# Kernel tuning notes

Hardware: AMD Instinct MI355X
Metric: run time of the kernel (lower is better)

Reference implementation:

```python
import jax, jax.numpy as jnp
import numpy as np

N = 100000
E = 1600000
D_IN, D_HID, D_OUT = 64, 64, 64
NEG_SLOPE = 0.2
EPS = 1e-16


def _gat_layer(x, W, att_src, att_dst, bias, src, dst, n_nodes):
    """Single-head PyG GATConv, add_self_loops=False."""
    h = x @ W                                  # [N, out]
    a_s = h @ att_src                          # [N] per-node source score
    a_d = h @ att_dst                          # [N] per-node dest score
    e = jax.nn.leaky_relu(a_s[src] + a_d[dst], NEG_SLOPE)   # [E]
    # softmax over incoming edges of each dst node
    m = jax.ops.segment_max(e, dst, num_segments=n_nodes)    # [N]
    ex = jnp.exp(e - m[dst])                                  # [E]
    denom = jax.ops.segment_sum(ex, dst, num_segments=n_nodes)  # [N]
    alpha = ex / (denom[dst] + EPS)                            # [E]
    # weighted scatter-aggregate of source features to dst
    out = jax.ops.segment_sum(h[src] * alpha[:, None], dst, num_segments=n_nodes)
    return out + bias


def setup_inputs() -> dict:
    key = jax.random.key(0)
    ks = jax.random.split(key, 10)
    x = jax.random.normal(ks[0], (N, D_IN), dtype=jnp.float32)
    edge_index = jax.random.randint(ks[1], (2, E), 0, N, dtype=jnp.int32)
    s1 = 1.0 / np.sqrt(D_IN)
    s2 = 1.0 / np.sqrt(D_HID)
    return {
        "x": x,
        "edge_index": edge_index,
        "W1": jax.random.normal(ks[2], (D_IN, D_HID), dtype=jnp.float32) * s1,
        "att_src1": jax.random.normal(ks[3], (D_HID,), dtype=jnp.float32) * s2,
        "att_dst1": jax.random.normal(ks[4], (D_HID,), dtype=jnp.float32) * s2,
        "b1": jnp.zeros((D_HID,), dtype=jnp.float32),
        "W2": jax.random.normal(ks[5], (D_HID, D_OUT), dtype=jnp.float32) * s2,
        "att_src2": jax.random.normal(ks[6], (D_OUT,), dtype=jnp.float32) * (1.0 / np.sqrt(D_OUT)),
        "att_dst2": jax.random.normal(ks[7], (D_OUT,), dtype=jnp.float32) * (1.0 / np.sqrt(D_OUT)),
        "b2": jnp.zeros((D_OUT,), dtype=jnp.float32),
    }


def reference(x, edge_index, W1, att_src1, att_dst1, b1, W2, att_src2, att_dst2, b2):
    src, dst = edge_index[0], edge_index[1]
    h = _gat_layer(x, W1, att_src1, att_dst1, b1, src, dst, N)
    h = jax.nn.relu(h)
    # dropout(p=0.2) is identity in eval mode
    out = _gat_layer(h, W2, att_src2, att_dst2, b2, src, dst, N)
    return out
```

## Files before the change

### kernel.cpp

```cpp
#include <hip/hip_runtime.h>

#define N_NODES 100000
#define N_EDGES 1600000
#define D 64
#define NEG_SLOPE 0.2f
#define SM_EPS 1e-16f

#define BSHIFT 9
#define BSIZE (1 << BSHIFT)
#define NB ((N_NODES + BSIZE - 1) >> BSHIFT)
#define PAD 16
#define TPB 256
#define EPT 16
#define TILE (TPB * EPT)
#define NWG_E ((N_EDGES + TILE - 1) / TILE)
#define CSR_CAP 10240

#define GEMM_RR 8
#define GEMM_ROWS 128
#define NWG_GEMM ((N_NODES + GEMM_ROWS - 1) / GEMM_ROWS)

#define COMP(v, kk) ((kk) == 0 ? (v).x : (kk) == 1 ? (v).y : (kk) == 2 ? (v).z : (v).w)

typedef _Float16 half4_t __attribute__((ext_vector_type(4)));


__global__ __launch_bounds__(TPB) void k_bhist(const int* __restrict__ dst,
                                               int* __restrict__ gbh) {
    __shared__ int hist[NB];
    int t = threadIdx.x;
    for (int i = t; i < NB; i += TPB) hist[i] = 0;
    __syncthreads();
    int base = blockIdx.x * TILE;
#pragma unroll
    for (int j = 0; j < EPT; j++) {
        int i = base + j * TPB + t;
        if (i < N_EDGES) atomicAdd(&hist[dst[i] >> BSHIFT], 1);
    }
    __syncthreads();
    for (int i = t; i < NB; i += TPB)
        if (hist[i]) atomicAdd(&gbh[i * PAD], hist[i]);
}

__global__ __launch_bounds__(256) void k_scan_nb(const int* __restrict__ gbh,
                                                 int* __restrict__ bbase,
                                                 int* __restrict__ bcur) {
    __shared__ int lds[256];
    int t = threadIdx.x;
    int v = (t < NB) ? gbh[t * PAD] : 0;
    lds[t] = v;
    __syncthreads();
    for (int s = 1; s < 256; s <<= 1) {
        int a = (t >= s) ? lds[t - s] : 0;
        __syncthreads();
        lds[t] += a;
        __syncthreads();
    }
    int excl = lds[t] - v;
    if (t < NB) { bbase[t] = excl; bcur[t * PAD] = excl; }
    if (t == 0) bbase[NB] = N_EDGES;
}

__global__ __launch_bounds__(TPB) void k_bscatter(const int* __restrict__ src,
                                                  const int* __restrict__ dst,
                                                  int* __restrict__ bcur,
                                                  unsigned* __restrict__ ebuf) {
    __shared__ int hist[NB];
    __shared__ int cursor[NB];
    __shared__ int lbase[NB];
    __shared__ int tsum[TPB];
    __shared__ unsigned stage[TILE];
    __shared__ int stageaddr[TILE];
    int t = threadIdx.x;
    for (int i = t; i < NB; i += TPB) hist[i] = 0;
    __syncthreads();
    int base = blockIdx.x * TILE;
#pragma unroll
    for (int j = 0; j < EPT; j++) {
        int i = base + j * TPB + t;
        if (i < N_EDGES) atomicAdd(&hist[dst[i] >> BSHIFT], 1);
    }
    __syncthreads();
    int v = (t < NB) ? hist[t] : 0;
    tsum[t] = v;
    __syncthreads();
    for (int s = 1; s < 256; s <<= 1) {
        int a = (t >= s) ? tsum[t - s] : 0;
        __syncthreads();
        tsum[t] += a;
        __syncthreads();
    }
    int excl = tsum[t] - v;
    if (t < NB) {
        int gb = v ? atomicAdd(&bcur[t * PAD], v) : 0;
        lbase[t] = gb - excl;
        cursor[t] = excl;
    }
    __syncthreads();
#pragma unroll
    for (int j = 0; j < EPT; j++) {
        int i = base + j * TPB + t;
        if (i < N_EDGES) {
            int d = dst[i];
            int b = d >> BSHIFT;
            int r = atomicAdd(&cursor[b], 1);
            stage[r] = (unsigned)src[i] | ((unsigned)(d & (BSIZE - 1)) << 17);
            stageaddr[r] = lbase[b] + r;
        }
    }
    __syncthreads();
    int total = min(TILE, N_EDGES - base);
    for (int s = t; s < total; s += TPB) ebuf[stageaddr[s]] = stage[s];
}

__global__ __launch_bounds__(TPB) void k_bcsr(const int* __restrict__ bbase,
                                              const unsigned* __restrict__ ebuf,
                                              int* __restrict__ off,
                                              int* __restrict__ csr) {
    __shared__ int dh[BSIZE];
    __shared__ int dl[BSIZE];
    __shared__ int tsum[TPB];
    __shared__ int stage[CSR_CAP];
    int b = blockIdx.x;
    int t = threadIdx.x;
    int beg = bbase[b], end = bbase[b + 1];
    int cnt = end - beg;
    dh[t] = 0; dh[t + TPB] = 0;
    __syncthreads();
    for (int i = beg + t; i < end; i += TPB)
        atomicAdd(&dh[(ebuf[i] >> 17) & (BSIZE - 1)], 1);
    __syncthreads();
    int v0 = dh[2 * t], v1 = dh[2 * t + 1];
    tsum[t] = v0 + v1;
    __syncthreads();
    for (int s = 1; s < 256; s <<= 1) {
        int a = (t >= s) ? tsum[t - s] : 0;
        __syncthreads();
        tsum[t] += a;
        __syncthreads();
    }
    int excl = tsum[t] - (v0 + v1);
    dl[2 * t] = excl;
    dl[2 * t + 1] = excl + v0;
    int gd = (b << BSHIFT) + 2 * t;
    if (gd < N_NODES) off[gd] = beg + excl;
    if (gd + 1 < N_NODES) off[gd + 1] = beg + excl + v0;
    if (b == 0 && t == 0) off[N_NODES] = N_EDGES;
    dh[2 * t] = 0; dh[2 * t + 1] = 0;
    __syncthreads();
    if (cnt <= CSR_CAP) {
        for (int i = beg + t; i < end; i += TPB) {
            unsigned pk = ebuf[i];
            int ld = (pk >> 17) & (BSIZE - 1);
            int r = atomicAdd(&dh[ld], 1);
            stage[dl[ld] + r] = (int)(pk & 0x1FFFFu);
        }
        __syncthreads();
        for (int s = t; s < cnt; s += TPB) csr[beg + s] = stage[s];
    } else {
        for (int i = beg + t; i < end; i += TPB) {
            unsigned pk = ebuf[i];
            int ld = (pk >> 17) & (BSIZE - 1);
            int r = atomicAdd(&dh[ld], 1);
            csr[beg + dl[ld] + r] = (int)(pk & 0x1FFFFu);
        }
    }
}


__global__ __launch_bounds__(256) void k_wvec(
    const float* __restrict__ W1, const float* __restrict__ as1,
    const float* __restrict__ ad1, const float* __restrict__ W2,
    const float* __restrict__ as2, const float* __restrict__ ad2,
    float* __restrict__ wv) {
    int w = threadIdx.x >> 6, lane = threadIdx.x & 63;
    const float* W  = (w < 2) ? W1 : W2;
    const float* av = (w == 0) ? as1 : (w == 1) ? ad1 : (w == 2) ? as2 : ad2;
    const float4* Wr = (const float4*)(W + lane * D);
    const float4* a4 = (const float4*)av;
    float acc0 = 0.f, acc1 = 0.f;
#pragma unroll
    for (int c = 0; c < D / 8; c++) {
        float4 w0 = Wr[2 * c], w1 = Wr[2 * c + 1];
        float4 v0 = a4[2 * c], v1 = a4[2 * c + 1];
        acc0 += w0.x * v0.x + w0.y * v0.y + w0.z * v0.z + w0.w * v0.w;
        acc1 += w1.x * v1.x + w1.y * v1.y + w1.z * v1.z + w1.w * v1.w;
    }
    wv[w * D + lane] = acc0 + acc1;
}

__global__ __launch_bounds__(256) void k_gemm(
    const float* __restrict__ x, const float* __restrict__ W,
    const float* __restrict__ wv,
    _Float16* __restrict__ h16, float* __restrict__ a_s,
    float* __restrict__ a_d) {
    __shared__ float4 Wl4[D * D / 4];
    __shared__ float4 wvs[D / 4], wvd[D / 4];
    int t = threadIdx.x;
    const float4* W4 = (const float4*)W;
#pragma unroll
    for (int i = 0; i < 4; i++) Wl4[i * 256 + t] = W4[i * 256 + t];
    if (t < D / 4) wvs[t] = ((const float4*)wv)[t];
    else if (t < D / 2) wvd[t - D / 4] = ((const float4*)(wv + D))[t - D / 4];
    __syncthreads();
    int q = t & 15;
    int r0 = blockIdx.x * GEMM_ROWS + (t >> 4) * GEMM_RR;
    const float4* x4 = (const float4*)x;
    float4 acc[GEMM_RR];
    float sa[GEMM_RR], ea[GEMM_RR];
#pragma unroll
    for (int j = 0; j < GEMM_RR; j++) {
        acc[j] = {0.f, 0.f, 0.f, 0.f};
        sa[j] = 0.f; ea[j] = 0.f;
    }
    for (int k4 = 0; k4 < D / 4; k4++) {
        float4 ws4 = wvs[k4], wd4 = wvd[k4];
        float4 xv[GEMM_RR];
#pragma unroll
        for (int j = 0; j < GEMM_RR; j++) {
            int r = r0 + j;
            r = (r < N_NODES) ? r : N_NODES - 1;
            xv[j] = x4[(size_t)r * (D / 4) + k4];
        }
#pragma unroll
        for (int j = 0; j < GEMM_RR; j++) {
            sa[j] += xv[j].x * ws4.x + xv[j].y * ws4.y +
                     xv[j].z * ws4.z + xv[j].w * ws4.w;
            ea[j] += xv[j].x * wd4.x + xv[j].y * wd4.y +
                     xv[j].z * wd4.z + xv[j].w * wd4.w;
        }
#pragma unroll
        for (int kk = 0; kk < 4; kk++) {
            float4 w4 = Wl4[(k4 * 4 + kk) * 16 + q];
#pragma unroll
            for (int j = 0; j < GEMM_RR; j++) {
                float xs = COMP(xv[j], kk);
                acc[j].x = fmaf(xs, w4.x, acc[j].x);
                acc[j].y = fmaf(xs, w4.y, acc[j].y);
                acc[j].z = fmaf(xs, w4.z, acc[j].z);
                acc[j].w = fmaf(xs, w4.w, acc[j].w);
            }
        }
    }
#pragma unroll
    for (int j = 0; j < GEMM_RR; j++) {
        int r = r0 + j;
        if (r < N_NODES) {
            half4_t hh = {(_Float16)acc[j].x, (_Float16)acc[j].y,
                          (_Float16)acc[j].z, (_Float16)acc[j].w};
            *(half4_t*)(h16 + (size_t)r * D + q * 4) = hh;
            if (q == 0) { a_s[r] = sa[j]; a_d[r] = ea[j]; }
        }
    }
}

__global__ __launch_bounds__(256) void k_aggr(
    const int* __restrict__ off, const int* __restrict__ csr,
    const _Float16* __restrict__ h16, const float* __restrict__ a_s,
    const float* __restrict__ a_d, const float* __restrict__ bias,
    float* __restrict__ out, int do_relu) {
    int node = (blockIdx.x * blockDim.x + threadIdx.x) >> 4;
    int q = threadIdx.x & 15;
    if (node >= N_NODES) return;
    int beg = off[node], end = off[node + 1];
    float ad = a_d[node];
    float s = 0.f;
    float4 acc = {0.f, 0.f, 0.f, 0.f};
    for (int c = beg; c < end; c += 8) {
        int v[8];
        float w[8];
        half4_t hv[8];
#pragma unroll
        for (int i = 0; i < 8; i++) {
            int idx = c + i;
            v[i] = (idx < end) ? csr[idx] : csr[beg];
        }
#pragma unroll
        for (int i = 0; i < 8; i++)
            hv[i] = *(const half4_t*)(h16 + (size_t)v[i] * D + q * 4);
#pragma unroll
        for (int i = 0; i < 8; i++) {
            float tv = a_s[v[i]] + ad;
            tv = fmaxf(tv, NEG_SLOPE * tv);
            w[i] = (c + i < end) ? __expf(tv) : 0.f;
        }
#pragma unroll
        for (int i = 0; i < 8; i++) {
            s += w[i];
            acc.x = fmaf(w[i], (float)hv[i].x, acc.x);
            acc.y = fmaf(w[i], (float)hv[i].y, acc.y);
            acc.z = fmaf(w[i], (float)hv[i].z, acc.z);
            acc.w = fmaf(w[i], (float)hv[i].w, acc.w);
        }
    }
    float inv = 1.f / (s + SM_EPS);
    float4 b4 = ((const float4*)bias)[q];
    float4 o;
    o.x = fmaf(acc.x, inv, b4.x);
    o.y = fmaf(acc.y, inv, b4.y);
    o.z = fmaf(acc.z, inv, b4.z);
    o.w = fmaf(acc.w, inv, b4.w);
    if (do_relu) {
        o.x = fmaxf(o.x, 0.f); o.y = fmaxf(o.y, 0.f);
        o.z = fmaxf(o.z, 0.f); o.w = fmaxf(o.w, 0.f);
    }
    ((float4*)(out + (size_t)node * D))[q] = o;
}


extern "C" void kernel_launch(void* const* d_in, const int* in_sizes, int n_in,
                              void* d_out, int out_size, void* d_ws, size_t ws_size,
                              hipStream_t stream) {
    const float* x   = (const float*)d_in[0];
    const int*   ei  = (const int*)d_in[1];
    const float* W1  = (const float*)d_in[2];
    const float* as1 = (const float*)d_in[3];
    const float* ad1 = (const float*)d_in[4];
    const float* b1  = (const float*)d_in[5];
    const float* W2  = (const float*)d_in[6];
    const float* as2 = (const float*)d_in[7];
    const float* ad2 = (const float*)d_in[8];
    const float* b2  = (const float*)d_in[9];
    float* out = (float*)d_out;

    const int* src = ei;
    const int* dst = ei + N_EDGES;

    char* ws = (char*)d_ws;
    size_t o = 0;
    auto alloc = [&](size_t bytes) { void* p = ws + o; o += (bytes + 255) & ~255ull; return p; };
    _Float16* h16 = (_Float16*)alloc((size_t)N_NODES * D * sizeof(_Float16));
    float* a_s   = (float*)alloc(N_NODES * sizeof(float));
    float* a_d   = (float*)alloc(N_NODES * sizeof(float));
    int*   off   = (int*)alloc((N_NODES + 1) * sizeof(int));
    int*   csr   = (int*)alloc(N_EDGES * sizeof(int));
    int*   gbh   = (int*)alloc(NB * PAD * sizeof(int));
    int*   bbase = (int*)alloc((NB + 1) * sizeof(int));
    int*   bcur  = (int*)alloc(NB * PAD * sizeof(int));
    float* wv    = (float*)alloc(4 * D * sizeof(float));
    unsigned* ebuf = (unsigned*)h16;

    k_wvec<<<1, 256, 0, stream>>>(W1, as1, ad1, W2, as2, ad2, wv);

    hipMemsetAsync(gbh, 0, NB * PAD * sizeof(int), stream);
    k_bhist   <<<NWG_E, TPB, 0, stream>>>(dst, gbh);
    k_scan_nb <<<1, 256, 0, stream>>>(gbh, bbase, bcur);
    k_bscatter<<<NWG_E, TPB, 0, stream>>>(src, dst, bcur, ebuf);
    k_bcsr    <<<NB, TPB, 0, stream>>>(bbase, ebuf, off, csr);

    k_gemm<<<NWG_GEMM, 256, 0, stream>>>(x, W1, wv, h16, a_s, a_d);
    k_aggr<<<(N_NODES * 16 + 255) / 256, 256, 0, stream>>>(off, csr, h16, a_s, a_d, b1, out, 1);

    k_gemm<<<NWG_GEMM, 256, 0, stream>>>(out, W2, wv + 2 * D, h16, a_s, a_d);
    k_aggr<<<(N_NODES * 16 + 255) / 256, 256, 0, stream>>>(off, csr, h16, a_s, a_d, b2, out, 0);
}
```

Before: 278.4 us.

## Fuse layer-1 GEMM with edge histogram and widen CSR build blocks

The layer-1 GEMM and the destination-bucket histogram now run in one launch, with block ranges split between the two tasks. The separate attention-vector kernel goes away: each GEMM block computes W·att itself from the W tile already in shared memory. ebuf gets its own workspace buffer instead of aliasing h16, and the scatter and CSR kernels move from 256 to 512 threads per block. The aim is fewer launches and overlap of independent front-end work, at the cost of extra workspace memory and some redundant per-block dot products.

```diff
diff --git a/kernel.cpp b/kernel.cpp
--- a/kernel.cpp
+++ b/kernel.cpp
@@ -11,6 +11,7 @@
 #define NB ((N_NODES + BSIZE - 1) >> BSHIFT)
 #define PAD 16
 #define TPB 256
+#define TPB2 512
 #define EPT 16
 #define TILE (TPB * EPT)
 #define NWG_E ((N_EDGES + TILE - 1) / TILE)
@@ -24,188 +25,38 @@
 
 typedef _Float16 half4_t __attribute__((ext_vector_type(4)));
 
-
-__global__ __launch_bounds__(TPB) void k_bhist(const int* __restrict__ dst,
-                                               int* __restrict__ gbh) {
-    __shared__ int hist[NB];
-    int t = threadIdx.x;
-    for (int i = t; i < NB; i += TPB) hist[i] = 0;
-    __syncthreads();
-    int base = blockIdx.x * TILE;
-#pragma unroll
-    for (int j = 0; j < EPT; j++) {
-        int i = base + j * TPB + t;
-        if (i < N_EDGES) atomicAdd(&hist[dst[i] >> BSHIFT], 1);
-    }
-    __syncthreads();
-    for (int i = t; i < NB; i += TPB)
-        if (hist[i]) atomicAdd(&gbh[i * PAD], hist[i]);
-}
-
-__global__ __launch_bounds__(256) void k_scan_nb(const int* __restrict__ gbh,
-                                                 int* __restrict__ bbase,
-                                                 int* __restrict__ bcur) {
-    __shared__ int lds[256];
-    int t = threadIdx.x;
-    int v = (t < NB) ? gbh[t * PAD] : 0;
-    lds[t] = v;
-    __syncthreads();
-    for (int s = 1; s < 256; s <<= 1) {
-        int a = (t >= s) ? lds[t - s] : 0;
-        __syncthreads();
-        lds[t] += a;
-        __syncthreads();
-    }
-    int excl = lds[t] - v;
-    if (t < NB) { bbase[t] = excl; bcur[t * PAD] = excl; }
-    if (t == 0) bbase[NB] = N_EDGES;
-}
-
-__global__ __launch_bounds__(TPB) void k_bscatter(const int* __restrict__ src,
-                                                  const int* __restrict__ dst,
-                                                  int* __restrict__ bcur,
-                                                  unsigned* __restrict__ ebuf) {
-    __shared__ int hist[NB];
-    __shared__ int cursor[NB];
-    __shared__ int lbase[NB];
-    __shared__ int tsum[TPB];
-    __shared__ unsigned stage[TILE];
-    __shared__ int stageaddr[TILE];
-    int t = threadIdx.x;
-    for (int i = t; i < NB; i += TPB) hist[i] = 0;
-    __syncthreads();
-    int base = blockIdx.x * TILE;
-#pragma unroll
-    for (int j = 0; j < EPT; j++) {
-        int i = base + j * TPB + t;
-        if (i < N_EDGES) atomicAdd(&hist[dst[i] >> BSHIFT], 1);
-    }
-    __syncthreads();
-    int v = (t < NB) ? hist[t] : 0;
-    tsum[t] = v;
-    __syncthreads();
-    for (int s = 1; s < 256; s <<= 1) {
-        int a = (t >= s) ? tsum[t - s] : 0;
-        __syncthreads();
-        tsum[t] += a;
-        __syncthreads();
-    }
-    int excl = tsum[t] - v;
-    if (t < NB) {
-        int gb = v ? atomicAdd(&bcur[t * PAD], v) : 0;
-        lbase[t] = gb - excl;
-        cursor[t] = excl;
-    }
-    __syncthreads();
-#pragma unroll
-    for (int j = 0; j < EPT; j++) {
-        int i = base + j * TPB + t;
-        if (i < N_EDGES) {
-            int d = dst[i];
-            int b = d >> BSHIFT;
-            int r = atomicAdd(&cursor[b], 1);
-            stage[r] = (unsigned)src[i] | ((unsigned)(d & (BSIZE - 1)) << 17);
-            stageaddr[r] = lbase[b] + r;
-        }
-    }
-    __syncthreads();
-    int total = min(TILE, N_EDGES - base);
-    for (int s = t; s < total; s += TPB) ebuf[stageaddr[s]] = stage[s];
-}
-
-__global__ __launch_bounds__(TPB) void k_bcsr(const int* __restrict__ bbase,
-                                              const unsigned* __restrict__ ebuf,
-                                              int* __restrict__ off,
-                                              int* __restrict__ csr) {
-    __shared__ int dh[BSIZE];
-    __shared__ int dl[BSIZE];
-    __shared__ int tsum[TPB];
-    __shared__ int stage[CSR_CAP];
-    int b = blockIdx.x;
-    int t = threadIdx.x;
-    int beg = bbase[b], end = bbase[b + 1];
-    int cnt = end - beg;
-    dh[t] = 0; dh[t + TPB] = 0;
-    __syncthreads();
-    for (int i = beg + t; i < end; i += TPB)
-        atomicAdd(&dh[(ebuf[i] >> 17) & (BSIZE - 1)], 1);
-    __syncthreads();
-    int v0 = dh[2 * t], v1 = dh[2 * t + 1];
-    tsum[t] = v0 + v1;
-    __syncthreads();
-    for (int s = 1; s < 256; s <<= 1) {
-        int a = (t >= s) ? tsum[t - s] : 0;
-        __syncthreads();
-        tsum[t] += a;
-        __syncthreads();
-    }
-    int excl = tsum[t] - (v0 + v1);
-    dl[2 * t] = excl;
-    dl[2 * t + 1] = excl + v0;
-    int gd = (b << BSHIFT) + 2 * t;
-    if (gd < N_NODES) off[gd] = beg + excl;
-    if (gd + 1 < N_NODES) off[gd + 1] = beg + excl + v0;
-    if (b == 0 && t == 0) off[N_NODES] = N_EDGES;
-    dh[2 * t] = 0; dh[2 * t + 1] = 0;
-    __syncthreads();
-    if (cnt <= CSR_CAP) {
-        for (int i = beg + t; i < end; i += TPB) {
-            unsigned pk = ebuf[i];
-            int ld = (pk >> 17) & (BSIZE - 1);
-            int r = atomicAdd(&dh[ld], 1);
-            stage[dl[ld] + r] = (int)(pk & 0x1FFFFu);
-        }
-        __syncthreads();
-        for (int s = t; s < cnt; s += TPB) csr[beg + s] = stage[s];
-    } else {
-        for (int i = beg + t; i < end; i += TPB) {
-            unsigned pk = ebuf[i];
-            int ld = (pk >> 17) & (BSIZE - 1);
-            int r = atomicAdd(&dh[ld], 1);
-            csr[beg + dl[ld] + r] = (int)(pk & 0x1FFFFu);
-        }
-    }
-}
-
-
-__global__ __launch_bounds__(256) void k_wvec(
-    const float* __restrict__ W1, const float* __restrict__ as1,
-    const float* __restrict__ ad1, const float* __restrict__ W2,
-    const float* __restrict__ as2, const float* __restrict__ ad2,
-    float* __restrict__ wv) {
-    int w = threadIdx.x >> 6, lane = threadIdx.x & 63;
-    const float* W  = (w < 2) ? W1 : W2;
-    const float* av = (w == 0) ? as1 : (w == 1) ? ad1 : (w == 2) ? as2 : ad2;
-    const float4* Wr = (const float4*)(W + lane * D);
-    const float4* a4 = (const float4*)av;
-    float acc0 = 0.f, acc1 = 0.f;
-#pragma unroll
-    for (int c = 0; c < D / 8; c++) {
-        float4 w0 = Wr[2 * c], w1 = Wr[2 * c + 1];
-        float4 v0 = a4[2 * c], v1 = a4[2 * c + 1];
-        acc0 += w0.x * v0.x + w0.y * v0.y + w0.z * v0.z + w0.w * v0.w;
-        acc1 += w1.x * v1.x + w1.y * v1.y + w1.z * v1.z + w1.w * v1.w;
-    }
-    wv[w * D + lane] = acc0 + acc1;
-}
-
-__global__ __launch_bounds__(256) void k_gemm(
+__device__ __forceinline__ void gemm_block(
+    char* smraw, int bid,
     const float* __restrict__ x, const float* __restrict__ W,
-    const float* __restrict__ wv,
+    const float* __restrict__ att_s, const float* __restrict__ att_d,
     _Float16* __restrict__ h16, float* __restrict__ a_s,
     float* __restrict__ a_d) {
-    __shared__ float4 Wl4[D * D / 4];
-    __shared__ float4 wvs[D / 4], wvd[D / 4];
+    float4* Wl4 = (float4*)smraw;
+    float* wvs = (float*)(smraw + 16384);
+    float* wvd = wvs + D;
     int t = threadIdx.x;
     const float4* W4 = (const float4*)W;
 #pragma unroll
     for (int i = 0; i < 4; i++) Wl4[i * 256 + t] = W4[i * 256 + t];
-    if (t < D / 4) wvs[t] = ((const float4*)wv)[t];
-    else if (t < D / 2) wvd[t - D / 4] = ((const float4*)(wv + D))[t - D / 4];
+    __syncthreads();
+    if (t < 128) {
+        int row = t & 63;
+        const float4* a4 = (const float4*)((t < 64) ? att_s : att_d);
+        float s = 0.f;
+#pragma unroll
+        for (int q4 = 0; q4 < 16; q4++) {
+            float4 wr = Wl4[row * 16 + q4];
+            float4 aa = a4[q4];
+            s += wr.x * aa.x + wr.y * aa.y + wr.z * aa.z + wr.w * aa.w;
+        }
+        if (t < 64) wvs[row] = s; else wvd[row] = s;
+    }
     __syncthreads();
     int q = t & 15;
-    int r0 = blockIdx.x * GEMM_ROWS + (t >> 4) * GEMM_RR;
+    int r0 = bid * GEMM_ROWS + (t >> 4) * GEMM_RR;
     const float4* x4 = (const float4*)x;
+    const float4* wvs4 = (const float4*)wvs;
+    const float4* wvd4 = (const float4*)wvd;
     float4 acc[GEMM_RR];
     float sa[GEMM_RR], ea[GEMM_RR];
 #pragma unroll
@@ -214,7 +65,7 @@
         sa[j] = 0.f; ea[j] = 0.f;
     }
     for (int k4 = 0; k4 < D / 4; k4++) {
-        float4 ws4 = wvs[k4], wd4 = wvd[k4];
+        float4 ws4 = wvs4[k4], wd4 = wvd4[k4];
         float4 xv[GEMM_RR];
 #pragma unroll
         for (int j = 0; j < GEMM_RR; j++) {
@@ -253,6 +104,170 @@
         }
     }
 }
+
+__device__ __forceinline__ void bhist_block(
+    char* smraw, int bid, const int* __restrict__ dst, int* __restrict__ gbh) {
+    int* hist = (int*)smraw;
+    int t = threadIdx.x;
+    for (int i = t; i < NB; i += TPB) hist[i] = 0;
+    __syncthreads();
+    int base = bid * TILE;
+#pragma unroll
+    for (int j = 0; j < EPT; j++) {
+        int i = base + j * TPB + t;
+        if (i < N_EDGES) atomicAdd(&hist[dst[i] >> BSHIFT], 1);
+    }
+    __syncthreads();
+    for (int i = t; i < NB; i += TPB)
+        if (hist[i]) atomicAdd(&gbh[i * PAD], hist[i]);
+}
+
+__global__ __launch_bounds__(256) void k_front(
+    const float* __restrict__ x, const float* __restrict__ W1,
+    const float* __restrict__ as1, const float* __restrict__ ad1,
+    _Float16* __restrict__ h16, float* __restrict__ a_s,
+    float* __restrict__ a_d, const int* __restrict__ dst,
+    int* __restrict__ gbh) {
+    __shared__ __align__(16) char smraw[16896];
+    if (blockIdx.x < NWG_GEMM)
+        gemm_block(smraw, blockIdx.x, x, W1, as1, ad1, h16, a_s, a_d);
+    else
+        bhist_block(smraw, blockIdx.x - NWG_GEMM, dst, gbh);
+}
+
+__global__ __launch_bounds__(256) void k_gemm2(
+    const float* __restrict__ x, const float* __restrict__ W,
+    const float* __restrict__ att_s, const float* __restrict__ att_d,
+    _Float16* __restrict__ h16, float* __restrict__ a_s,
+    float* __restrict__ a_d) {
+    __shared__ __align__(16) char smraw[16896];
+    gemm_block(smraw, blockIdx.x, x, W, att_s, att_d, h16, a_s, a_d);
+}
+
+
+__global__ __launch_bounds__(256) void k_scan_nb(const int* __restrict__ gbh,
+                                                 int* __restrict__ bbase,
+                                                 int* __restrict__ bcur) {
+    __shared__ int lds[256];
+    int t = threadIdx.x;
+    int v = (t < NB) ? gbh[t * PAD] : 0;
+    lds[t] = v;
+    __syncthreads();
+    for (int s = 1; s < 256; s <<= 1) {
+        int a = (t >= s) ? lds[t - s] : 0;
+        __syncthreads();
+        lds[t] += a;
+        __syncthreads();
+    }
+    int excl = lds[t] - v;
+    if (t < NB) { bbase[t] = excl; bcur[t * PAD] = excl; }
+    if (t == 0) bbase[NB] = N_EDGES;
+}
+
+__global__ __launch_bounds__(TPB2) void k_bscatter(const int* __restrict__ src,
+                                                   const int* __restrict__ dst,
+                                                   int* __restrict__ bcur,
+                                                   unsigned* __restrict__ ebuf) {
+    __shared__ int hist[NB];
+    __shared__ int cursor[NB];
+    __shared__ int lbase[NB];
+    __shared__ int tsum[TPB2];
+    __shared__ unsigned stage[TILE];
+    __shared__ int stageaddr[TILE];
+    int t = threadIdx.x;
+    for (int i = t; i < NB; i += TPB2) hist[i] = 0;
+    __syncthreads();
+    int base = blockIdx.x * TILE;
+#pragma unroll
+    for (int j = 0; j < TILE / TPB2; j++) {
+        int i = base + j * TPB2 + t;
+        if (i < N_EDGES) atomicAdd(&hist[dst[i] >> BSHIFT], 1);
+    }
+    __syncthreads();
+    int v = (t < NB) ? hist[t] : 0;
+    tsum[t] = v;
+    __syncthreads();
+    for (int s = 1; s < TPB2; s <<= 1) {
+        int a = (t >= s) ? tsum[t - s] : 0;
+        __syncthreads();
+        tsum[t] += a;
+        __syncthreads();
+    }
+    int excl = tsum[t] - v;
+    if (t < NB) {
+        int gb = v ? atomicAdd(&bcur[t * PAD], v) : 0;
+        lbase[t] = gb - excl;
+        cursor[t] = excl;
+    }
+    __syncthreads();
+#pragma unroll
+    for (int j = 0; j < TILE / TPB2; j++) {
+        int i = base + j * TPB2 + t;
+        if (i < N_EDGES) {
+            int d = dst[i];
+            int b = d >> BSHIFT;
+            int r = atomicAdd(&cursor[b], 1);
+            stage[r] = (unsigned)src[i] | ((unsigned)(d & (BSIZE - 1)) << 17);
+            stageaddr[r] = lbase[b] + r;
+        }
+    }
+    __syncthreads();
+    int total = min(TILE, N_EDGES - base);
+    for (int s = t; s < total; s += TPB2) ebuf[stageaddr[s]] = stage[s];
+}
+
+__global__ __launch_bounds__(TPB2) void k_bcsr(const int* __restrict__ bbase,
+                                               const unsigned* __restrict__ ebuf,
+                                               int* __restrict__ off,
+                                               int* __restrict__ csr) {
+    __shared__ int dh[BSIZE];
+    __shared__ int dl[BSIZE];
+    __shared__ int tsum[TPB2];
+    __shared__ int stage[CSR_CAP];
+    int b = blockIdx.x;
+    int t = threadIdx.x;
+    int beg = bbase[b], end = bbase[b + 1];
+    int cnt = end - beg;
+    dh[t] = 0;
+    __syncthreads();
+    for (int i = beg + t; i < end; i += TPB2)
+        atomicAdd(&dh[(ebuf[i] >> 17) & (BSIZE - 1)], 1);
+    __syncthreads();
+    int v = dh[t];
+    tsum[t] = v;
+    __syncthreads();
+    for (int s = 1; s < TPB2; s <<= 1) {
+        int a = (t >= s) ? tsum[t - s] : 0;
+        __syncthreads();
+        tsum[t] += a;
+        __syncthreads();
+    }
+    int excl = tsum[t] - v;
+    dl[t] = excl;
+    int gd = (b << BSHIFT) + t;
+    if (gd < N_NODES) off[gd] = beg + excl;
+    if (b == 0 && t == 0) off[N_NODES] = N_EDGES;
+    dh[t] = 0;
+    __syncthreads();
+    if (cnt <= CSR_CAP) {
+        for (int i = beg + t; i < end; i += TPB2) {
+            unsigned pk = ebuf[i];
+            int ld = (pk >> 17) & (BSIZE - 1);
+            int r = atomicAdd(&dh[ld], 1);
+            stage[dl[ld] + r] = (int)(pk & 0x1FFFFu);
+        }
+        __syncthreads();
+        for (int s = t; s < cnt; s += TPB2) csr[beg + s] = stage[s];
+    } else {
+        for (int i = beg + t; i < end; i += TPB2) {
+            unsigned pk = ebuf[i];
+            int ld = (pk >> 17) & (BSIZE - 1);
+            int r = atomicAdd(&dh[ld], 1);
+            csr[beg + dl[ld] + r] = (int)(pk & 0x1FFFFu);
+        }
+    }
+}
+
 
 __global__ __launch_bounds__(256) void k_aggr(
     const int* __restrict__ off, const int* __restrict__ csr,
@@ -330,6 +345,7 @@
     size_t o = 0;
     auto alloc = [&](size_t bytes) { void* p = ws + o; o += (bytes + 255) & ~255ull; return p; };
     _Float16* h16 = (_Float16*)alloc((size_t)N_NODES * D * sizeof(_Float16));
+    unsigned* ebuf = (unsigned*)alloc(N_EDGES * sizeof(unsigned));
     float* a_s   = (float*)alloc(N_NODES * sizeof(float));
     float* a_d   = (float*)alloc(N_NODES * sizeof(float));
     int*   off   = (int*)alloc((N_NODES + 1) * sizeof(int));
@@ -337,20 +353,16 @@
     int*   gbh   = (int*)alloc(NB * PAD * sizeof(int));
     int*   bbase = (int*)alloc((NB + 1) * sizeof(int));
     int*   bcur  = (int*)alloc(NB * PAD * sizeof(int));
-    float* wv    = (float*)alloc(4 * D * sizeof(float));
-    unsigned* ebuf = (unsigned*)h16;
-
-    k_wvec<<<1, 256, 0, stream>>>(W1, as1, ad1, W2, as2, ad2, wv);
 
     hipMemsetAsync(gbh, 0, NB * PAD * sizeof(int), stream);
-    k_bhist   <<<NWG_E, TPB, 0, stream>>>(dst, gbh);
+    k_front<<<NWG_GEMM + NWG_E, 256, 0, stream>>>(x, W1, as1, ad1, h16, a_s, a_d, dst, gbh);
+
     k_scan_nb <<<1, 256, 0, stream>>>(gbh, bbase, bcur);
-    k_bscatter<<<NWG_E, TPB, 0, stream>>>(src, dst, bcur, ebuf);
-    k_bcsr    <<<NB, TPB, 0, stream>>>(bbase, ebuf, off, csr);
-
-    k_gemm<<<NWG_GEMM, 256, 0, stream>>>(x, W1, wv, h16, a_s, a_d);
+    k_bscatter<<<NWG_E, TPB2, 0, stream>>>(src, dst, bcur, ebuf);
+    k_bcsr    <<<NB, TPB2, 0, stream>>>(bbase, ebuf, off, csr);
+
     k_aggr<<<(N_NODES * 16 + 255) / 256, 256, 0, stream>>>(off, csr, h16, a_s, a_d, b1, out, 1);
 
-    k_gemm<<<NWG_GEMM, 256, 0, stream>>>(out, W2, wv + 2 * D, h16, a_s, a_d);
+    k_gemm2<<<NWG_GEMM, 256, 0, stream>>>(out, W2, as2, ad2, h16, a_s, a_d);
     k_aggr<<<(N_NODES * 16 + 255) / 256, 256, 0, stream>>>(off, csr, h16, a_s, a_d, b2, out, 0);
 }
```

Result: faster. 255.9 us (-8.1%).
